# Kernel tuning notes

Hardware: AMD Instinct MI355X
Metric: run time of the kernel (lower is better)

The kernel has to match this reference:

```python
import jax, jax.numpy as jnp
import numpy as np

B, N, C = 4, 2048, 81
IMG_W, IMG_H = 1024.0, 800.0
SCORE_THRESH = 0.05
NMS_THRESH = 0.5
DETS_PER_IMG = 100
BBOX_XFORM_CLIP = float(np.log(1000.0 / 16.0))
WX, WY, WW, WH = 10.0, 10.0, 5.0, 5.0


def _make_boxes(key, n):
    k1, k2, k3, k4 = jax.random.split(key, 4)
    x1 = jax.random.uniform(k1, (n,)) * (IMG_W - 60.0)
    y1 = jax.random.uniform(k2, (n,)) * (IMG_H - 60.0)
    w = 10.0 + jax.random.uniform(k3, (n,)) * 300.0
    h = 10.0 + jax.random.uniform(k4, (n,)) * 300.0
    return jnp.stack([x1, y1, jnp.minimum(x1 + w, IMG_W - 1.0), jnp.minimum(y1 + h, IMG_H - 1.0)], axis=-1)


def setup_inputs() -> dict:
    key = jax.random.key(0)
    k1, k2, k3, k4 = jax.random.split(key, 4)
    return {
        "class_logits": jax.random.normal(k1, (B * N, C), jnp.float32),
        "box_regression": jax.random.normal(k2, (B * N, C * 8), jnp.float32) * 0.5,
        "left_proposals": _make_boxes(k3, B * N),
        "right_proposals": _make_boxes(k4, B * N),
    }


def decode(rel, boxes):
    widths = boxes[:, 2] - boxes[:, 0] + 1.0
    heights = boxes[:, 3] - boxes[:, 1] + 1.0
    ctr_x = boxes[:, 0] + 0.5 * widths
    ctr_y = boxes[:, 1] + 0.5 * heights
    dx = rel[:, 0::4] / WX
    dy = rel[:, 1::4] / WY
    dw = jnp.minimum(rel[:, 2::4] / WW, BBOX_XFORM_CLIP)
    dh = jnp.minimum(rel[:, 3::4] / WH, BBOX_XFORM_CLIP)
    pcx = dx * widths[:, None] + ctr_x[:, None]
    pcy = dy * heights[:, None] + ctr_y[:, None]
    pw = jnp.exp(dw) * widths[:, None]
    ph = jnp.exp(dh) * heights[:, None]
    x1 = pcx - 0.5 * pw
    y1 = pcy - 0.5 * ph
    x2 = pcx + 0.5 * pw - 1.0
    y2 = pcy + 0.5 * ph - 1.0
    return jnp.stack([x1, y1, x2, y2], axis=-1)  # [M, C, 4]


def clip_boxes(b):
    x1 = jnp.clip(b[..., 0], 0.0, IMG_W - 1.0)
    y1 = jnp.clip(b[..., 1], 0.0, IMG_H - 1.0)
    x2 = jnp.clip(b[..., 2], 0.0, IMG_W - 1.0)
    y2 = jnp.clip(b[..., 3], 0.0, IMG_H - 1.0)
    return jnp.stack([x1, y1, x2, y2], axis=-1)


def pairwise_iou(b):
    area = jnp.clip(b[:, 2] - b[:, 0] + 1.0, 0.0) * jnp.clip(b[:, 3] - b[:, 1] + 1.0, 0.0)
    lt = jnp.maximum(b[:, None, :2], b[None, :, :2])
    rb = jnp.minimum(b[:, None, 2:], b[None, :, 2:])
    wh = jnp.clip(rb - lt + 1.0, 0.0)
    inter = wh[..., 0] * wh[..., 1]
    return inter / jnp.maximum(area[:, None] + area[None, :] - inter, 1e-6)


def nms_keep(boxes, scores):
    # greedy NMS -> boolean keep mask (fixed shape)
    n = scores.shape[0]
    order = jnp.argsort(-scores)
    iou = pairwise_iou(boxes[order])
    idx = jnp.arange(n)
    def body(i, keep):
        sup = (iou[i] > NMS_THRESH) & keep[i] & (idx > i)
        return keep & (~sup)
    keep = jax.lax.fori_loop(0, n, body, jnp.ones((n,), bool))
    return jnp.zeros((n,), bool).at[order].set(keep)


def _per_image(prob, lb, rb):
    # prob [N,C], lb/rb [N,C,4]
    labels = jnp.argmax(prob, axis=-1)
    ar = jnp.arange(prob.shape[0])
    score = prob[ar, labels]
    lbox = lb[ar, labels]
    rbox = rb[ar, labels]
    valid = (labels >= 1) & (score > SCORE_THRESH)
    s = jnp.where(valid, score, -jnp.inf)
    keep = nms_keep(lbox, s) & nms_keep(rbox, s) & valid
    ms = jnp.where(keep, score, -jnp.inf)
    kth = jax.lax.top_k(ms, DETS_PER_IMG)[0][-1]
    keep = keep & (ms >= kth)
    return lbox, rbox, score, keep


def reference(class_logits, box_regression, left_proposals, right_proposals):
    prob = jax.nn.softmax(class_logits, axis=-1)  # [B*N, C]
    reg = box_regression.reshape(-1, C, 8)
    lb = clip_boxes(decode(reg[:, :, :4].reshape(-1, C * 4), left_proposals))
    rb = clip_boxes(decode(reg[:, :, 4:].reshape(-1, C * 4), right_proposals))
    prob = prob.reshape(B, N, C)
    lb = lb.reshape(B, N, C, 4)
    rb = rb.reshape(B, N, C, 4)
    lbox, rbox, score, keep = jax.vmap(_per_image)(prob, lb, rb)
    m = keep[..., None].astype(score.dtype)
    out = jnp.concatenate([lbox * m, rbox * m, jnp.where(keep, score, 0.0)[..., None]], axis=-1)
    return out  # [B, N, 9]
```

## Files before the change

kernel.cpp:

```cpp
#include <hip/hip_runtime.h>
#include <math.h>

#define NPROP 2048
#define NIMG 4
#define NCLS 81
#define REGW 648
#define SCORE_THRESH 0.05f
#define NMS_T 0.5f
#define DETS 100
#define XC 1023.0f
#define YC 799.0f
#define BBOX_CLIP 4.135166556742356f
#define NBIN 8192
#define SEL 320
#define MAXC 512
#define WRD 8
#define TRIP 2560

typedef unsigned long long u64;

__device__ __forceinline__ float areaf(float4 v) {
  return fmaxf(v.z - v.x + 1.0f, 0.0f) * fmaxf(v.w - v.y + 1.0f, 0.0f);
}
__device__ __forceinline__ bool iou_gt(float4 a, float aa, float4 b, float ba) {
  float ix1 = fmaxf(a.x, b.x), iy1 = fmaxf(a.y, b.y);
  float ix2 = fminf(a.z, b.z), iy2 = fminf(a.w, b.w);
  float iw = fmaxf(ix2 - ix1 + 1.0f, 0.0f);
  float ih = fmaxf(iy2 - iy1 + 1.0f, 0.0f);
  float inter = iw * ih;
  return inter > NMS_T * fmaxf(aa + ba - inter, 1e-6f);
}
__device__ __forceinline__ float score_from_v(unsigned v) {
  unsigned uu = ~v;
  unsigned bits = (uu & 0x80000000u) ? (uu & 0x7fffffffu) : ~uu;
  return __uint_as_float(bits);
}
__device__ __forceinline__ float4 decode_side(const float* __restrict__ reg,
                                              const float4* __restrict__ props,
                                              int grow, int ci, int isR) {
  const float* r = reg + (size_t)grow * REGW + ci * 8 + isR * 4;
  float4 P = props[grow];
  float w  = P.z - P.x + 1.0f;
  float h  = P.w - P.y + 1.0f;
  float cx = P.x + 0.5f * w;
  float cy = P.y + 0.5f * h;
  float dx = r[0] / 10.0f;
  float dy = r[1] / 10.0f;
  float dw = fminf(r[2] / 5.0f, BBOX_CLIP);
  float dh = fminf(r[3] / 5.0f, BBOX_CLIP);
  float pcx = dx * w + cx;
  float pcy = dy * h + cy;
  float pw = expf(dw) * w;
  float ph = expf(dh) * h;
  float4 o;
  o.x = fminf(fmaxf(pcx - 0.5f * pw, 0.0f), XC);
  o.y = fminf(fmaxf(pcy - 0.5f * ph, 0.0f), YC);
  o.z = fminf(fmaxf(pcx + 0.5f * pw - 1.0f, 0.0f), XC);
  o.w = fminf(fmaxf(pcy + 0.5f * ph - 1.0f, 0.0f), YC);
  return o;
}

__global__ __launch_bounds__(256) void score_kernel(
    const float* __restrict__ logits,
    unsigned* __restrict__ v32G, unsigned short* __restrict__ ci16G) {
  int row  = blockIdx.x * 4 + (threadIdx.x >> 6);
  int lane = threadIdx.x & 63;
  const float* lr = logits + (size_t)row * NCLS;
  float a = lr[lane];
  float b = (lane < NCLS - 64) ? lr[lane + 64] : -INFINITY;
  float v; int ci;
  if (b > a) { v = b; ci = lane + 64; } else { v = a; ci = lane; }
  for (int o = 32; o; o >>= 1) {
    float ov = __shfl_xor(v, o);
    int   oc = __shfl_xor(ci, o);
    if (ov > v || (ov == v && oc < ci)) { v = ov; ci = oc; }
  }
  float e = expf(a - v) + ((lane < NCLS - 64) ? expf(b - v) : 0.0f);
  for (int o = 32; o; o >>= 1) e += __shfl_xor(e, o);
  if (lane == 0) {
    float score = 1.0f / e;
    unsigned vv = 0xFFFFFFFFu;
    if (ci >= 1 && score > SCORE_THRESH) {
      unsigned uu = __float_as_uint(score);
      uu = (uu & 0x80000000u) ? ~uu : (uu | 0x80000000u);
      vv = ~uu;
    }
    v32G[row]  = vv;
    ci16G[row] = (unsigned short)ci;
  }
}

__global__ __launch_bounds__(1024) void select_kernel(
    const unsigned* __restrict__ v32G,
    unsigned short* __restrict__ srowG, unsigned* __restrict__ svG,
    int* __restrict__ C1G, int* __restrict__ C2G, int* __restrict__ flagG) {
  __shared__ int hist[NBIN];
  __shared__ u64 keys[MAXC];
  __shared__ int wsum[16];
  __shared__ int Ts, cnts, ovf;
  int b = blockIdx.x, tid = threadIdx.x, ln = tid & 63, w = tid >> 6;
  const unsigned* v32 = v32G + b * NPROP;
  if (tid == 0) { Ts = NBIN - 1; cnts = 0; ovf = 0; }
  for (int i = tid; i < NBIN; i += 1024) hist[i] = 0;
  __syncthreads();
  for (int p = tid; p < NPROP; p += 1024) {
    unsigned v = v32[p];
    if (v != 0xFFFFFFFFu) atomicAdd(&hist[v >> 19], 1);
  }
  __syncthreads();
  {
    int base = tid * 8;
    int c[8]; int acc = 0;
#pragma unroll
    for (int k = 0; k < 8; ++k) { acc += hist[base + k]; c[k] = acc; }
    int tot = acc, v = tot;
#pragma unroll
    for (int o = 1; o < 64; o <<= 1) { int n = __shfl_up(v, o); if (ln >= o) v += n; }
    if (ln == 63) wsum[w] = v;
    __syncthreads();
    if (tid < 16) {
      int x = wsum[tid];
#pragma unroll
      for (int o = 1; o < 16; o <<= 1) { int n = __shfl_up(x, o); if (tid >= o) x += n; }
      wsum[tid] = x;
    }
    __syncthreads();
    int incl = ((w > 0) ? wsum[w - 1] : 0) + v;
    int off = incl - tot;
    int prev = off;
#pragma unroll
    for (int k = 0; k < 8; ++k) {
      int cur = off + c[k];
      if (cur >= SEL && prev < SEL) Ts = base + k;
      prev = cur;
    }
  }
  __syncthreads();
  int T = Ts, nvTot = wsum[15];
  for (int p = tid; p < NPROP; p += 1024) {
    unsigned v = v32[p];
    bool cand = (v != 0xFFFFFFFFu) && ((int)(v >> 19) <= T);
    u64 mb = __ballot(cand);
    int lpos = (int)__popcll(mb & ((1ull << ln) - 1ull));
    int wb = 0;
    if (ln == 0 && mb) wb = atomicAdd(&cnts, (int)__popcll(mb));
    wb = __shfl(wb, 0);
    if (cand) {
      int dst = wb + lpos;
      if (dst < MAXC) keys[dst] = ((u64)v << 16) | (unsigned)p;
      else ovf = 1;
    }
  }
  __syncthreads();
  int C1 = cnts;
  if (C1 > MAXC || ovf) {
    if (tid == 0) { flagG[b] = 1; C1G[b] = 0; C2G[b] = nvTot; }
    return;
  }
  if (tid < 256) {
    int i0 = tid, i1 = tid + 256;
    u64 k0 = (i0 < C1) ? keys[i0] : ~0ull;
    u64 k1 = (i1 < C1) ? keys[i1] : ~0ull;
    int r0 = 0, r1 = 0;
#pragma unroll 4
    for (int j = 0; j < C1; ++j) {
      u64 kj = keys[j];
      r0 += (kj < k0) ? 1 : 0;
      r1 += (kj < k1) ? 1 : 0;
    }
    if (i0 < C1) { srowG[b * MAXC + r0] = (unsigned short)(k0 & 0xFFFFull);
                   svG[b * MAXC + r0]   = (unsigned)(k0 >> 16); }
    if (i1 < C1) { srowG[b * MAXC + r1] = (unsigned short)(k1 & 0xFFFFull);
                   svG[b * MAXC + r1]   = (unsigned)(k1 >> 16); }
  }
  if (tid == 0) { flagG[b] = 0; C1G[b] = C1; C2G[b] = nvTot; }
}

__global__ __launch_bounds__(256) void prep_kernel(
    const float* __restrict__ reg, const float* __restrict__ lp,
    const float* __restrict__ rp, const unsigned short* __restrict__ ci16G,
    const unsigned short* __restrict__ srowG, const int* __restrict__ C1G,
    const int* __restrict__ flagG, float* __restrict__ out,
    float4* __restrict__ bxLG, float4* __restrict__ bxRG) {
  int g = blockIdx.x * 256 + threadIdx.x;
  float4 z4 = make_float4(0.f, 0.f, 0.f, 0.f);
  ((float4*)out)[g] = z4;
  if (g < NIMG * MAXC) {
    int b = g >> 9, pos = g & (MAXC - 1);
    float4 L = z4, R = z4;
    if (flagG[b] == 0 && pos < C1G[b]) {
      int row  = srowG[b * MAXC + pos];
      int grow = b * NPROP + row;
      int ci   = ci16G[grow];
      L = decode_side(reg, (const float4*)lp, grow, ci, 0);
      R = decode_side(reg, (const float4*)rp, grow, ci, 1);
    }
    bxLG[g] = L; bxRG[g] = R;
  }
}

__global__ __launch_bounds__(1024) void build_kernel(
    const float4* __restrict__ bxLG, const float4* __restrict__ bxRG,
    const int* __restrict__ C1G, const int* __restrict__ flagG,
    u64* __restrict__ keepLG, u64* __restrict__ keepRG) {
  __shared__ float4 bx[MAXC];
  __shared__ u64    mat[TRIP];
  __shared__ int C1_s, flag_s;
  int b = blockIdx.x >> 1, side = blockIdx.x & 1;
  int tid = threadIdx.x, ln = tid & 63, w = tid >> 6;
  if (tid == 0) { C1_s = C1G[b]; flag_s = flagG[b]; }
  __syncthreads();
  if (flag_s) return;
  int C1 = C1_s;
  if (C1 == 0) return;
  int WRDu = (C1 + 63) >> 6;
  const float4* src = (side ? bxRG : bxLG) + b * MAXC;
  if (tid < MAXC) bx[tid] = src[tid];
  __syncthreads();

  {
    int rb = w & 7, part = w >> 3;
    int r = rb * 64 + ln;
    float4 rbx = bx[r];
    float  rar = areaf(rbx);
    int tb = 0;
    for (int k = 0; k < rb; ++k) tb += ((8 - k) | 1);
    int Sw = (8 - rb) | 1;
    u64* myrow = &mat[tb * 64 + ln * Sw];
    for (int cw = rb + part; cw < WRDu; cw += 2) {
      u64 m = 0;
      const float4* cp = &bx[cw * 64];
#pragma unroll 8
      for (int c = 0; c < 64; ++c) {
        float4 cb = cp[c];
        float car = areaf(cb);
        if (iou_gt(rbx, rar, cb, car)) m |= (1ull << c);
      }
      if (cw == rb) m &= ~((2ull << ln) - 1ull);
      myrow[cw - rb] = m;
    }
  }
  __syncthreads();

  if (w == 0) {
    u64 A[WRD];
#pragma unroll
    for (int t = 0; t < WRD; ++t) {
      int b0 = t * 64;
      A[t] = (C1 >= b0 + 64) ? ~0ull : (C1 > b0 ? ((1ull << (C1 - b0)) - 1ull) : 0ull);
    }
    int tbase = 0;
#pragma unroll
    for (int wb = 0; wb < WRD; ++wb) {
      if (wb * 64 < C1) {
        const int Sw = (8 - wb) | 1;
        const u64* rowp = &mat[tbase];
        u64 aw = A[wb];
#pragma unroll
        for (int g = 0; g < 4; ++g) {
          u64 d[16];
#pragma unroll
          for (int k = 0; k < 16; ++k) d[k] = rowp[(g * 16 + k) * Sw];
#pragma unroll
          for (int k = 0; k < 16; ++k) {
            u64 msk = 0ull - ((aw >> (g * 16 + k)) & 1ull);
            aw &= ~(msk & d[k]);
          }
        }
        A[wb] = aw;
        bool alive = (aw >> ln) & 1ull;
#pragma unroll
        for (int t = wb + 1; t < WRD; ++t) {
          if (t * 64 < C1) {
            u64 x = alive ? rowp[ln * Sw + (t - wb)] : 0ull;
#pragma unroll
            for (int o = 1; o < 64; o <<= 1)
              x |= __shfl_xor((unsigned long long)x, o);
            A[t] &= ~x;
          }
        }
      }
      tbase += 64 * ((8 - wb) | 1);
    }
    if (ln == 0) {
      u64* kG = (side ? keepRG : keepLG) + b * WRD;
#pragma unroll
      for (int t = 0; t < WRD; ++t)
        if (t * 64 < C1) kG[t] = A[t];
    }
  }
}

struct SN {
  u64 keys[NPROP];
  unsigned short sidx[NPROP];
  unsigned v32s[NPROP];
  float4 bxL[MAXC], bxR[MAXC];
  float  arL[MAXC], arR[MAXC];
  u64 keepbL[NPROP / 64], keepbR[NPROP / 64];
  u64 rowmL[64], rowmR[64];
  float4 cbL[64], cbR[64];
  float  cbLa[64], cbRa[64];
  u64 aL, aR;
  int cnt, prevCount, done, ccL, ccR, needFB;
  unsigned kthV;
};

__device__ __forceinline__ float4 get_sboxN(SN* S, const float* reg,
                                            const float4* lp4, const float4* rp4,
                                            const unsigned short* ci16G,
                                            int b, int pos, int isR) {
  if (pos < MAXC) return isR ? S->bxR[pos] : S->bxL[pos];
  int row = S->sidx[pos];
  int grow = b * NPROP + row;
  return decode_side(reg, isR ? rp4 : lp4, grow, ci16G[grow], isR);
}

__global__ __launch_bounds__(1024) void finale_fallback_kernel(
    const float* __restrict__ reg, const float* __restrict__ lp,
    const float* __restrict__ rp, const unsigned* __restrict__ v32G,
    const unsigned short* __restrict__ ci16G,
    const u64* __restrict__ keepLG, const u64* __restrict__ keepRG,
    const unsigned* __restrict__ svG, const unsigned short* __restrict__ srowG,
    const float4* __restrict__ bxLG, const float4* __restrict__ bxRG,
    const int* __restrict__ C1G, const int* __restrict__ C2G,
    float* __restrict__ out) {
  __shared__ SN S;
  int b = blockIdx.x, tid = threadIdx.x, ln = tid & 63, w = tid >> 6;
  float* ob = out + (size_t)b * NPROP * 9;

  if (w == 0) {
    int C1 = C1G[b];
    int before = 0;
    unsigned kth = 0;
    for (int wb = 0; wb * 64 < C1; ++wb) {
      u64 m = keepLG[b * WRD + wb] & keepRG[b * WRD + wb];
      int pos = wb * 64 + ln;
      bool bit = (m >> ln) & 1ull;
      int rank = before + (int)__popcll(m & ((1ull << ln) - 1ull));
      unsigned vA = svG[b * MAXC + pos];
      u64 selm = __ballot(bit && rank == DETS - 1);
      if (selm) kth = __shfl(vA, __ffsll(selm) - 1);
      bool qual = bit && (rank < DETS || vA == kth);
      if (qual) {
        int row = srowG[b * MAXC + pos];
        float4 L = bxLG[b * MAXC + pos], R = bxRG[b * MAXC + pos];
        float* orow = ob + row * 9;
        orow[0]=L.x; orow[1]=L.y; orow[2]=L.z; orow[3]=L.w;
        orow[4]=R.x; orow[5]=R.y; orow[6]=R.z; orow[7]=R.w;
        orow[8]=score_from_v(vA);
      }
      before += (int)__popcll(m);
    }
    if (ln == 0) {
      S.needFB = (before < DETS && C2G[b] > C1) ? 1 : 0;
      S.cnt = 0; S.prevCount = 0; S.done = 0; S.kthV = 0u;
    }
  }
  __syncthreads();
  if (!S.needFB) return;

  const float4* lp4 = (const float4*)lp;
  const float4* rp4 = (const float4*)rp;
  float4* ob4 = (float4*)ob;
  float4 z4 = make_float4(0.f, 0.f, 0.f, 0.f);
  for (int i = tid; i < NPROP * 9 / 4; i += 1024) ob4[i] = z4;
  for (int p = tid; p < NPROP; p += 1024) {
    unsigned v = v32G[b * NPROP + p];
    S.v32s[p] = v;
    bool cand = (v != 0xFFFFFFFFu);
    u64 mb = __ballot(cand);
    int lpos = (int)__popcll(mb & ((1ull << ln) - 1ull));
    int wb = 0;
    if (ln == 0 && mb) wb = atomicAdd(&S.cnt, (int)__popcll(mb));
    wb = __shfl(wb, 0);
    if (cand) S.keys[wb + lpos] = ((u64)v << 16) | (unsigned)p;
  }
  __syncthreads();
  int C2 = S.cnt;
  int CbEnd = (C2 + 63) & ~63;
  {
    int i0 = tid, i1 = tid + 1024;
    u64 k0 = (i0 < C2) ? S.keys[i0] : ~0ull;
    u64 k1 = (i1 < C2) ? S.keys[i1] : ~0ull;
    int r0 = 0, r1 = 0;
#pragma unroll 4
    for (int j = 0; j < C2; ++j) {
      u64 kj = S.keys[j];
      r0 += (kj < k0) ? 1 : 0;
      r1 += (kj < k1) ? 1 : 0;
    }
    if (i0 < C2) S.sidx[r0] = (unsigned short)(k0 & 0xFFFFull);
    if (i1 < C2) S.sidx[r1] = (unsigned short)(k1 & 0xFFFFull);
  }
  for (int i = C2 + tid; i < CbEnd; i += 1024) S.sidx[i] = 0;
  for (int wd = tid; wd < NPROP / 64; wd += 1024) {
    int b0 = wd << 6;
    u64 mf = 0ull;
    if (C2 >= b0 + 64) mf = ~0ull;
    else if (C2 > b0)  mf = (1ull << (C2 - b0)) - 1ull;
    S.keepbL[wd] = mf; S.keepbR[wd] = mf;
  }
  __syncthreads();
  {
    int lim = min(CbEnd, MAXC);
    for (int i = tid; i < lim; i += 1024) {
      if (i < C2) {
        int row = S.sidx[i];
        int grow = b * NPROP + row;
        int ci = ci16G[grow];
        float4 L = decode_side(reg, lp4, grow, ci, 0);
        float4 R = decode_side(reg, rp4, grow, ci, 1);
        S.bxL[i] = L; S.arL[i] = areaf(L);
        S.bxR[i] = R; S.arR[i] = areaf(R);
      } else {
        S.bxL[i] = z4; S.arL[i] = 1.0f;
        S.bxR[i] = z4; S.arR[i] = 1.0f;
      }
    }
  }
  __syncthreads();
  for (int base = 0; base < CbEnd; base += 64) {
    {
      int isR = (w >= 8);
      float4 cbx = get_sboxN(&S, reg, lp4, rp4, ci16G, b, base + ln, isR);
      float car = (base + ln < MAXC) ? (isR ? S.arR[base + ln] : S.arL[base + ln])
                                     : areaf(cbx);
      int w8 = w & 7;
#pragma unroll
      for (int k = 0; k < 8; ++k) {
        int row = w8 * 8 + k;
        float4 rbx;
        rbx.x = __shfl(cbx.x, row); rbx.y = __shfl(cbx.y, row);
        rbx.z = __shfl(cbx.z, row); rbx.w = __shfl(cbx.w, row);
        float rar = __shfl(car, row);
        bool bit = (ln > row) && iou_gt(rbx, rar, cbx, car);
        u64 bal = __ballot(bit);
        if (ln == 0) { if (isR) S.rowmR[row] = bal; else S.rowmL[row] = bal; }
      }
    }
    __syncthreads();
    if (tid < 128) {
      int isR = (tid >= 64);
      u64* km = isR ? S.keepbR : S.keepbL;
      u64* rm = isR ? S.rowmR  : S.rowmL;
      u64 a = km[base >> 6];
#pragma unroll
      for (int j = 0; j < 64; ++j)
        a &= ~((0ull - ((a >> j) & 1ull)) & rm[j]);
      if (ln == 0) {
        km[base >> 6] = a;
        if (isR) { S.aR = a; S.ccR = __popcll(a); }
        else     { S.aL = a; S.ccL = __popcll(a); }
      }
      if ((a >> ln) & 1ull) {
        int pos = __popcll(a & ((1ull << ln) - 1ull));
        float4 v = get_sboxN(&S, reg, lp4, rp4, ci16G, b, base + ln, isR);
        if (isR) { S.cbR[pos] = v; S.cbRa[pos] = areaf(v); }
        else     { S.cbL[pos] = v; S.cbLa[pos] = areaf(v); }
      }
    }
    __syncthreads();
    if (w == 0) {
      u64 m = S.aL & S.aR;
      int before = S.prevCount;
      bool bit = (m >> ln) & 1ull;
      int rank = before + (int)__popcll(m & ((1ull << ln) - 1ull));
      int row = S.sidx[base + ln];
      unsigned vA = S.v32s[row];
      u64 selm = __ballot(bit && rank == DETS - 1);
      unsigned keffV = S.kthV;
      if (selm) keffV = __shfl(vA, __ffsll(selm) - 1);
      bool qual = bit && (rank < DETS || vA == keffV);
      if (qual) {
        float4 L = get_sboxN(&S, reg, lp4, rp4, ci16G, b, base + ln, 0);
        float4 R = get_sboxN(&S, reg, lp4, rp4, ci16G, b, base + ln, 1);
        float s = score_from_v(vA);
        float* orow = ob + row * 9;
        orow[0]=L.x; orow[1]=L.y; orow[2]=L.z; orow[3]=L.w;
        orow[4]=R.x; orow[5]=R.y; orow[6]=R.z; orow[7]=R.w;
        orow[8]=s;
      }
      if (ln == 0) {
        if (selm) S.kthV = keffV;
        int nc = before + (int)__popcll(m);
        S.prevCount = nc;
        if (nc >= DETS) {
          int nxt = base + 64;
          bool cont = false;
          if (nxt < C2) cont = (S.v32s[S.sidx[nxt]] == keffV);
          if (!cont) S.done = 1;
        }
      }
    } else {
      int cL = S.ccL, cR = S.ccR;
      if ((cL | cR) != 0) {
        for (int p = base + 64 + (tid - 64); p < CbEnd; p += 960) {
          float4 mbL = get_sboxN(&S, reg, lp4, rp4, ci16G, b, p, 0);
          float al = (p < MAXC) ? S.arL[p] : areaf(mbL);
          bool supL = false;
          for (int q = 0; q < cL; ++q)
            supL = supL || iou_gt(mbL, al, S.cbL[q], S.cbLa[q]);
          if (supL) atomicAnd(&S.keepbL[p >> 6], ~(1ull << (p & 63)));
          float4 mbR = get_sboxN(&S, reg, lp4, rp4, ci16G, b, p, 1);
          float ar_ = (p < MAXC) ? S.arR[p] : areaf(mbR);
          bool supR = false;
          for (int q = 0; q < cR; ++q)
            supR = supR || iou_gt(mbR, ar_, S.cbR[q], S.cbRa[q]);
          if (supR) atomicAnd(&S.keepbR[p >> 6], ~(1ull << (p & 63)));
        }
      }
    }
    __syncthreads();
    if (S.done) break;
  }
}

extern "C" void kernel_launch(void* const* d_in, const int* in_sizes, int n_in,
                              void* d_out, int out_size, void* d_ws, size_t ws_size,
                              hipStream_t stream) {
  const float* logits = (const float*)d_in[0];
  const float* reg    = (const float*)d_in[1];
  const float* lprop  = (const float*)d_in[2];
  const float* rprop  = (const float*)d_in[3];
  float* out = (float*)d_out;

  char* ws = (char*)d_ws;
  unsigned*       v32G   = (unsigned*)(ws + 0);
  unsigned short* ci16G  = (unsigned short*)(ws + 32768);
  unsigned short* srowG  = (unsigned short*)(ws + 49152);
  unsigned*       svG    = (unsigned*)(ws + 53248);
  float4*         bxLG   = (float4*)(ws + 61440);
  float4*         bxRG   = (float4*)(ws + 94208);
  u64*            keepLG = (u64*)(ws + 126976);
  u64*            keepRG = (u64*)(ws + 127232);
  int*            C1G    = (int*)(ws + 127488);
  int*            C2G    = (int*)(ws + 127504);
  int*            flagG  = (int*)(ws + 127520);

  score_kernel  <<<NIMG * NPROP / 4, 256,  0, stream>>>(logits, v32G, ci16G);
  select_kernel <<<NIMG,             1024, 0, stream>>>(v32G, srowG, svG, C1G, C2G, flagG);
  prep_kernel   <<<72,               256,  0, stream>>>(reg, lprop, rprop, ci16G, srowG,
                                                        C1G, flagG, out, bxLG, bxRG);
  build_kernel  <<<2 * NIMG,         1024, 0, stream>>>(bxLG, bxRG, C1G, flagG,
                                                        keepLG, keepRG);
  finale_fallback_kernel<<<NIMG,     1024, 0, stream>>>(reg, lprop, rprop, v32G, ci16G,
                                                        keepLG, keepRG, svG, srowG,
                                                        bxLG, bxRG, C1G, C2G, out);
}
```

Measured before the change: 129.6 us.

## Fuse select, prep and build kernels into one per-side NMS kernel

Merges the candidate selection, box decode and IoU-matrix build into a single kernel launched once per image and side, and moves output zeroing into the score kernel. This removes two kernel launches and the global round trips through srow and the decoded boxes between stages. In exchange the selection histogram and rank sort are computed twice per image (once per side block), and two blocks write the same srow/sv/C1/flag values redundantly. Shared memory per block grows because hist, keys, bx and mat now coexist.

```diff
diff --git a/kernel.cpp b/kernel.cpp
--- a/kernel.cpp
+++ b/kernel.cpp
@@ -62,9 +62,14 @@
 
 __global__ __launch_bounds__(256) void score_kernel(
     const float* __restrict__ logits,
-    unsigned* __restrict__ v32G, unsigned short* __restrict__ ci16G) {
+    unsigned* __restrict__ v32G, unsigned short* __restrict__ ci16G,
+    float* __restrict__ out) {
   int row  = blockIdx.x * 4 + (threadIdx.x >> 6);
   int lane = threadIdx.x & 63;
+  if (blockIdx.x < 72) {
+    int g = blockIdx.x * 256 + threadIdx.x;
+    ((float4*)out)[g] = make_float4(0.f, 0.f, 0.f, 0.f);
+  }
   const float* lr = logits + (size_t)row * NCLS;
   float a = lr[lane];
   float b = (lane < NCLS - 64) ? lr[lane + 64] : -INFINITY;
@@ -90,15 +95,23 @@
   }
 }
 
-__global__ __launch_bounds__(1024) void select_kernel(
-    const unsigned* __restrict__ v32G,
+__global__ __launch_bounds__(1024) void nms8_kernel(
+    const unsigned* __restrict__ v32G, const unsigned short* __restrict__ ci16G,
+    const float* __restrict__ reg, const float* __restrict__ lp,
+    const float* __restrict__ rp,
     unsigned short* __restrict__ srowG, unsigned* __restrict__ svG,
+    float4* __restrict__ bxLG, float4* __restrict__ bxRG,
+    u64* __restrict__ keepLG, u64* __restrict__ keepRG,
     int* __restrict__ C1G, int* __restrict__ C2G, int* __restrict__ flagG) {
   __shared__ int hist[NBIN];
   __shared__ u64 keys[MAXC];
+  __shared__ unsigned short ssort[MAXC];
+  __shared__ float4 bx[MAXC];
+  __shared__ u64 mat[TRIP];
   __shared__ int wsum[16];
   __shared__ int Ts, cnts, ovf;
-  int b = blockIdx.x, tid = threadIdx.x, ln = tid & 63, w = tid >> 6;
+  int b = blockIdx.x >> 1, side = blockIdx.x & 1;
+  int tid = threadIdx.x, ln = tid & 63, w = tid >> 6;
   const unsigned* v32 = v32G + b * NPROP;
   if (tid == 0) { Ts = NBIN - 1; cnts = 0; ovf = 0; }
   for (int i = tid; i < NBIN; i += 1024) hist[i] = 0;
@@ -157,6 +170,7 @@
     if (tid == 0) { flagG[b] = 1; C1G[b] = 0; C2G[b] = nvTot; }
     return;
   }
+  if (tid == 0) { flagG[b] = 0; C1G[b] = C1; C2G[b] = nvTot; }
   if (tid < 256) {
     int i0 = tid, i1 = tid + 256;
     u64 k0 = (i0 < C1) ? keys[i0] : ~0ull;
@@ -168,54 +182,33 @@
       r0 += (kj < k0) ? 1 : 0;
       r1 += (kj < k1) ? 1 : 0;
     }
-    if (i0 < C1) { srowG[b * MAXC + r0] = (unsigned short)(k0 & 0xFFFFull);
-                   svG[b * MAXC + r0]   = (unsigned)(k0 >> 16); }
-    if (i1 < C1) { srowG[b * MAXC + r1] = (unsigned short)(k1 & 0xFFFFull);
-                   svG[b * MAXC + r1]   = (unsigned)(k1 >> 16); }
-  }
-  if (tid == 0) { flagG[b] = 0; C1G[b] = C1; C2G[b] = nvTot; }
-}
-
-__global__ __launch_bounds__(256) void prep_kernel(
-    const float* __restrict__ reg, const float* __restrict__ lp,
-    const float* __restrict__ rp, const unsigned short* __restrict__ ci16G,
-    const unsigned short* __restrict__ srowG, const int* __restrict__ C1G,
-    const int* __restrict__ flagG, float* __restrict__ out,
-    float4* __restrict__ bxLG, float4* __restrict__ bxRG) {
-  int g = blockIdx.x * 256 + threadIdx.x;
-  float4 z4 = make_float4(0.f, 0.f, 0.f, 0.f);
-  ((float4*)out)[g] = z4;
-  if (g < NIMG * MAXC) {
-    int b = g >> 9, pos = g & (MAXC - 1);
-    float4 L = z4, R = z4;
-    if (flagG[b] == 0 && pos < C1G[b]) {
-      int row  = srowG[b * MAXC + pos];
+    if (i0 < C1) {
+      unsigned short rw = (unsigned short)(k0 & 0xFFFFull);
+      ssort[r0] = rw;
+      srowG[b * MAXC + r0] = rw;
+      svG[b * MAXC + r0]   = (unsigned)(k0 >> 16);
+    }
+    if (i1 < C1) {
+      unsigned short rw = (unsigned short)(k1 & 0xFFFFull);
+      ssort[r1] = rw;
+      srowG[b * MAXC + r1] = rw;
+      svG[b * MAXC + r1]   = (unsigned)(k1 >> 16);
+    }
+  }
+  __syncthreads();
+
+  int WRDu = (C1 + 63) >> 6;
+  if (tid < MAXC) {
+    float4 B = make_float4(0.f, 0.f, 0.f, 0.f);
+    if (tid < C1) {
+      int row  = ssort[tid];
       int grow = b * NPROP + row;
       int ci   = ci16G[grow];
-      L = decode_side(reg, (const float4*)lp, grow, ci, 0);
-      R = decode_side(reg, (const float4*)rp, grow, ci, 1);
-    }
-    bxLG[g] = L; bxRG[g] = R;
-  }
-}
-
-__global__ __launch_bounds__(1024) void build_kernel(
-    const float4* __restrict__ bxLG, const float4* __restrict__ bxRG,
-    const int* __restrict__ C1G, const int* __restrict__ flagG,
-    u64* __restrict__ keepLG, u64* __restrict__ keepRG) {
-  __shared__ float4 bx[MAXC];
-  __shared__ u64    mat[TRIP];
-  __shared__ int C1_s, flag_s;
-  int b = blockIdx.x >> 1, side = blockIdx.x & 1;
-  int tid = threadIdx.x, ln = tid & 63, w = tid >> 6;
-  if (tid == 0) { C1_s = C1G[b]; flag_s = flagG[b]; }
-  __syncthreads();
-  if (flag_s) return;
-  int C1 = C1_s;
-  if (C1 == 0) return;
-  int WRDu = (C1 + 63) >> 6;
-  const float4* src = (side ? bxRG : bxLG) + b * MAXC;
-  if (tid < MAXC) bx[tid] = src[tid];
+      B = decode_side(reg, (const float4*)(side ? rp : lp), grow, ci, side);
+      (side ? bxRG : bxLG)[b * MAXC + tid] = B;
+    }
+    bx[tid] = B;
+  }
   __syncthreads();
 
   {
@@ -410,7 +403,7 @@
         int grow = b * NPROP + row;
         int ci = ci16G[grow];
         float4 L = decode_side(reg, lp4, grow, ci, 0);
-        float4 R = decode_side(reg, rp4, grow, ci, 1);
+        float4 R = decode_side(reg, lp4 == rp4 ? lp4 : rp4, grow, ci, 1);
         S.bxL[i] = L; S.arL[i] = areaf(L);
         S.bxR[i] = R; S.arR[i] = areaf(R);
       } else {
@@ -538,13 +531,11 @@
   int*            C2G    = (int*)(ws + 127504);
   int*            flagG  = (int*)(ws + 127520);
 
-  score_kernel  <<<NIMG * NPROP / 4, 256,  0, stream>>>(logits, v32G, ci16G);
-  select_kernel <<<NIMG,             1024, 0, stream>>>(v32G, srowG, svG, C1G, C2G, flagG);
-  prep_kernel   <<<72,               256,  0, stream>>>(reg, lprop, rprop, ci16G, srowG,
-                                                        C1G, flagG, out, bxLG, bxRG);
-  build_kernel  <<<2 * NIMG,         1024, 0, stream>>>(bxLG, bxRG, C1G, flagG,
-                                                        keepLG, keepRG);
-  finale_fallback_kernel<<<NIMG,     1024, 0, stream>>>(reg, lprop, rprop, v32G, ci16G,
-                                                        keepLG, keepRG, svG, srowG,
-                                                        bxLG, bxRG, C1G, C2G, out);
-}
+  score_kernel<<<NIMG * NPROP / 4, 256,  0, stream>>>(logits, v32G, ci16G, out);
+  nms8_kernel <<<2 * NIMG,         1024, 0, stream>>>(v32G, ci16G, reg, lprop, rprop,
+                                                      srowG, svG, bxLG, bxRG,
+                                                      keepLG, keepRG, C1G, C2G, flagG);
+  finale_fallback_kernel<<<NIMG,   1024, 0, stream>>>(reg, lprop, rprop, v32G, ci16G,
+                                                      keepLG, keepRG, svG, srowG,
+                                                      bxLG, bxRG, C1G, C2G, out);
+}
```

Measured after the change: 123.3 us. -4.9%, faster.
